# Kernel tuning notes

Measured on AMD Instinct MI355X. Metric: run time of the kernel, lower is better.

The kernel has to match this reference:

```python
import jax, jax.numpy as jnp
import numpy as np

IGNORE_INDEX = -100


def setup_inputs() -> dict:
    key = jax.random.key(0)
    k1, k2, k3 = jax.random.split(key, 3)
    N, H, V = 4096, 1024, 32000
    x = jax.random.normal(k1, (N, H), dtype=jnp.float32)
    # lm_head weight, laid out [H, V] so logits = x @ weight (kernel's [D, V] layout)
    weight = jax.random.normal(k2, (H, V), dtype=jnp.float32) * (1.0 / np.sqrt(H))
    target = jax.random.randint(k3, (N,), 0, V)
    # exercise the ignore_index masking path
    target = target.at[:64].set(IGNORE_INDEX)
    return {"x": x, "weight": weight, "target": target}


def reference(x, weight, target):
    # Fused linear + cross entropy, reduction='sum'.
    # logits: [N, V] (the tensor the fused kernel tiles to avoid materializing)
    logits = jnp.dot(x, weight)
    lse = jax.nn.logsumexp(logits, axis=-1)                  # [N]
    valid = target != IGNORE_INDEX                            # [N]
    safe_labels = jnp.where(valid, target, 0)
    target_logits = jnp.take_along_axis(logits, safe_labels[:, None], axis=-1)[:, 0]
    vmask = valid.astype(logits.dtype)
    losses = (lse - target_logits) * vmask                    # [N], 0 where ignored
    lse_masked = lse * vmask
    # reduction == 'sum'
    return losses.sum(), lse_masked.sum()
```

## Files before the change

### kernel.cpp

```cpp
#include <hip/hip_runtime.h>
#include <hip/hip_bf16.h>

typedef float f32x4 __attribute__((ext_vector_type(4)));
typedef int i32x4v __attribute__((ext_vector_type(4)));
typedef int i32x8v __attribute__((ext_vector_type(8)));

#define IGNORE_INDEX (-100)
#define N_ROWS 4096
#define H_DIM  1024
#define V_DIM  32000

#define BM 128
#define BN 128
#define BK 128
#define CT_NUM (V_DIM / BN)
#define RT_NUM (N_ROWS / BM)
#define SCALE1 0x7f7f7f7f

#define XB8 (N_ROWS * H_DIM / (256 * 16))
__global__ __launch_bounds__(256) void k_prep(const float* __restrict__ x,
                                              const float* __restrict__ w,
                                              unsigned char* __restrict__ x8,
                                              unsigned char* __restrict__ wT8) {
  __shared__ float tile[128][65];
  const int t = threadIdx.x;
  if (blockIdx.x < XB8) {
    size_t i = ((size_t)blockIdx.x * 256 + t) * 16;
    const float4* xp = (const float4*)(x + i);
    float4 f0 = xp[0], f1 = xp[1], f2 = xp[2], f3 = xp[3];
    int4 o;
    int r;
    r = __builtin_amdgcn_cvt_pk_fp8_f32(f0.x, f0.y, 0, false);
    r = __builtin_amdgcn_cvt_pk_fp8_f32(f0.z, f0.w, r, true);
    o.x = r;
    r = __builtin_amdgcn_cvt_pk_fp8_f32(f1.x, f1.y, 0, false);
    r = __builtin_amdgcn_cvt_pk_fp8_f32(f1.z, f1.w, r, true);
    o.y = r;
    r = __builtin_amdgcn_cvt_pk_fp8_f32(f2.x, f2.y, 0, false);
    r = __builtin_amdgcn_cvt_pk_fp8_f32(f2.z, f2.w, r, true);
    o.z = r;
    r = __builtin_amdgcn_cvt_pk_fp8_f32(f3.x, f3.y, 0, false);
    r = __builtin_amdgcn_cvt_pk_fp8_f32(f3.z, f3.w, r, true);
    o.w = r;
    *(int4*)(x8 + i) = o;
    return;
  }
  const int b = blockIdx.x - XB8;
  const int v0 = (b % (V_DIM / 64)) * 64;
  const int k0 = (b / (V_DIM / 64)) * 128;
  {
    const int vq = t & 15;
    const int kr = t >> 4;
#pragma unroll
    for (int p = 0; p < 128; p += 16) {
      float4 v = *(const float4*)(w + (size_t)(k0 + kr + p) * V_DIM + v0 + vq * 4);
      tile[kr + p][vq * 4 + 0] = v.x;
      tile[kr + p][vq * 4 + 1] = v.y;
      tile[kr + p][vq * 4 + 2] = v.z;
      tile[kr + p][vq * 4 + 3] = v.w;
    }
  }
  __syncthreads();
  {
    const int vr = t >> 2;
    const int kq2 = t & 3;
#pragma unroll
    for (int h = 0; h < 2; ++h) {
      const int d4 = kq2 + h * 4;
      int4 o;
      int r;
#pragma unroll
      for (int d = 0; d < 4; ++d) {
        r = __builtin_amdgcn_cvt_pk_fp8_f32(tile[d4 * 16 + d * 4 + 0][vr],
                                            tile[d4 * 16 + d * 4 + 1][vr], 0, false);
        r = __builtin_amdgcn_cvt_pk_fp8_f32(tile[d4 * 16 + d * 4 + 2][vr],
                                            tile[d4 * 16 + d * 4 + 3][vr], r, true);
        ((int*)&o)[d] = r;
      }
      *(int4*)(wT8 + (size_t)(v0 + vr) * H_DIM + k0 + d4 * 16) = o;
    }
  }
}

__global__ __launch_bounds__(256) void k_gemm_lse(const unsigned char* __restrict__ A,
                                                  const unsigned char* __restrict__ Bt,
                                                  float* __restrict__ m_part,
                                                  float* __restrict__ s_part) {
  __shared__ __align__(16) unsigned char sMem[2][2][BM * BK];
  float* maxbuf = (float*)&sMem[0][0][0];
  float* sumbuf = (float*)&sMem[0][0][2048];

  const int tid = threadIdx.x;
  const int rt = blockIdx.x;
  const int ct = blockIdx.y;
  const int m0 = rt * BM;
  const int n0 = ct * BN;

  const int w = tid >> 6;
  const int l = tid & 63;
  const int wr = w >> 1, wc = w & 1;
  const int quad = l >> 4, lc = l & 15;

  f32x4 acc[4][4];
#pragma unroll
  for (int i = 0; i < 4; ++i)
#pragma unroll
    for (int j = 0; j < 4; ++j)
      acc[i][j] = (f32x4){0.f, 0.f, 0.f, 0.f};

  const int srow = tid >> 3;
  const int scol = ((tid & 7) ^ ((tid >> 3) & 7)) * 16;
  const unsigned char* ga = A + (size_t)(m0 + srow) * H_DIM + scol;
  const unsigned char* gb = Bt + (size_t)(n0 + srow) * H_DIM + scol;
  const int dOff = tid * 16;

  const int base_r = lc * 128;
  const int sw0 = ((quad * 2) ^ (lc & 7)) * 16;
  const int sw1 = ((quad * 2 + 1) ^ (lc & 7)) * 16;

#define ISSUE_TILE(buf)                                                          \
  do {                                                                           \
    unsigned char* da_ = &sMem[buf][0][dOff];                                    \
    unsigned char* db_ = &sMem[buf][1][dOff];                                    \
    _Pragma("unroll")                                                            \
    for (int i_ = 0; i_ < 4; ++i_) {                                             \
      __builtin_amdgcn_global_load_lds(                                          \
          (const __attribute__((address_space(1))) void*)(ga + (size_t)i_ * 32 * H_DIM), \
          (__attribute__((address_space(3))) void*)(da_ + i_ * 4096), 16, 0, 0); \
      __builtin_amdgcn_global_load_lds(                                          \
          (const __attribute__((address_space(1))) void*)(gb + (size_t)i_ * 32 * H_DIM), \
          (__attribute__((address_space(3))) void*)(db_ + i_ * 4096), 16, 0, 0); \
    }                                                                            \
    ga += BK;                                                                    \
    gb += BK;                                                                    \
  } while (0)

  ISSUE_TILE(0);

#pragma unroll
  for (int kt = 0; kt < H_DIM / BK; ++kt) {
    __syncthreads();
    if (kt < H_DIM / BK - 1) ISSUE_TILE((kt + 1) & 1);

    const unsigned char* bufA = &sMem[kt & 1][0][0];
    const unsigned char* bufB = &sMem[kt & 1][1][0];
    i32x8v a_frag[4], b_frag[4];
#pragma unroll
    for (int i = 0; i < 4; ++i) {
      const unsigned char* p = bufA + (wr * 4 + i) * 2048 + base_r;
      i32x4v lo = *(const i32x4v*)(p + sw0);
      i32x4v hi = *(const i32x4v*)(p + sw1);
      a_frag[i] = __builtin_shufflevector(lo, hi, 0, 1, 2, 3, 4, 5, 6, 7);
    }
#pragma unroll
    for (int j = 0; j < 4; ++j) {
      const unsigned char* p = bufB + (wc * 4 + j) * 2048 + base_r;
      i32x4v lo = *(const i32x4v*)(p + sw0);
      i32x4v hi = *(const i32x4v*)(p + sw1);
      b_frag[j] = __builtin_shufflevector(lo, hi, 0, 1, 2, 3, 4, 5, 6, 7);
    }
#pragma unroll
    for (int i = 0; i < 4; ++i)
#pragma unroll
      for (int j = 0; j < 4; ++j)
        acc[i][j] = __builtin_amdgcn_mfma_scale_f32_16x16x128_f8f6f4(
            a_frag[i], b_frag[j], acc[i][j], 0, 0, 0, SCALE1, 0, SCALE1);
  }
#undef ISSUE_TILE

  float rmax[4][4];
#pragma unroll
  for (int i = 0; i < 4; ++i)
#pragma unroll
    for (int r = 0; r < 4; ++r) {
      float mx = fmaxf(fmaxf(acc[i][0][r], acc[i][1][r]),
                       fmaxf(acc[i][2][r], acc[i][3][r]));
#pragma unroll
      for (int off = 1; off < 16; off <<= 1)
        mx = fmaxf(mx, __shfl_xor(mx, off, 64));
      rmax[i][r] = mx;
    }
  __syncthreads();
  if (lc == 0) {
#pragma unroll
    for (int i = 0; i < 4; ++i)
#pragma unroll
      for (int r = 0; r < 4; ++r)
        maxbuf[(wr * 64 + i * 16 + quad * 4 + r) * 2 + wc] = rmax[i][r];
  }
  __syncthreads();
  float rowmax[4][4];
#pragma unroll
  for (int i = 0; i < 4; ++i)
#pragma unroll
    for (int r = 0; r < 4; ++r) {
      int row = wr * 64 + i * 16 + quad * 4 + r;
      rowmax[i][r] = fmaxf(maxbuf[row * 2], maxbuf[row * 2 + 1]);
    }
#pragma unroll
  for (int i = 0; i < 4; ++i)
#pragma unroll
    for (int r = 0; r < 4; ++r) {
      float s = __expf(acc[i][0][r] - rowmax[i][r]) + __expf(acc[i][1][r] - rowmax[i][r]) +
                __expf(acc[i][2][r] - rowmax[i][r]) + __expf(acc[i][3][r] - rowmax[i][r]);
#pragma unroll
      for (int off = 1; off < 16; off <<= 1)
        s += __shfl_xor(s, off, 64);
      if (lc == 0) sumbuf[(wr * 64 + i * 16 + quad * 4 + r) * 2 + wc] = s;
    }
  __syncthreads();
  if (wc == 0 && lc == 0) {
#pragma unroll
    for (int i = 0; i < 4; ++i)
#pragma unroll
      for (int r = 0; r < 4; ++r) {
        int row = wr * 64 + i * 16 + quad * 4 + r;
        size_t idx = (size_t)(m0 + row) * CT_NUM + ct;
        m_part[idx] = rowmax[i][r];
        s_part[idx] = sumbuf[row * 2] + sumbuf[row * 2 + 1];
      }
  }
}

__global__ __launch_bounds__(256) void k_combine(const float* __restrict__ x,
                                                 const unsigned char* __restrict__ wT8,
                                                 const int* __restrict__ target,
                                                 const float* __restrict__ m_part,
                                                 const float* __restrict__ s_part,
                                                 float* __restrict__ blk_part) {
  __shared__ float red[8];
  const int wv = threadIdx.x >> 6;
  const int row = blockIdx.x * 4 + wv;
  const int l = threadIdx.x & 63;
  float m = -INFINITY, s = 0.f;
  for (int ctb = l; ctb < CT_NUM; ctb += 64) {
    float mj = m_part[(size_t)row * CT_NUM + ctb];
    float sj = s_part[(size_t)row * CT_NUM + ctb];
    float M = fmaxf(m, mj);
    s = s * __expf(m - M) + sj * __expf(mj - M);
    m = M;
  }
#pragma unroll
  for (int off = 1; off < 64; off <<= 1) {
    float mo = __shfl_xor(m, off, 64);
    float so = __shfl_xor(s, off, 64);
    float M = fmaxf(m, mo);
    s = s * __expf(m - M) + so * __expf(mo - M);
    m = M;
  }
  float lse = m + logf(s);
  int tgt = target[row];
  bool valid = (tgt != IGNORE_INDEX);
  int st = valid ? tgt : 0;
  const float* xr = x + (size_t)row * H_DIM + l * 16;
  int4 wv4 = *(const int4*)(wT8 + (size_t)st * H_DIM + l * 16);
  float t = 0.f;
#define ACC_DW(dw, base)                                              \
  t += xr[base + 0] * __builtin_amdgcn_cvt_f32_fp8(dw, 0);            \
  t += xr[base + 1] * __builtin_amdgcn_cvt_f32_fp8(dw, 1);            \
  t += xr[base + 2] * __builtin_amdgcn_cvt_f32_fp8(dw, 2);            \
  t += xr[base + 3] * __builtin_amdgcn_cvt_f32_fp8(dw, 3);
  ACC_DW(wv4.x, 0)
  ACC_DW(wv4.y, 4)
  ACC_DW(wv4.z, 8)
  ACC_DW(wv4.w, 12)
#undef ACC_DW
#pragma unroll
  for (int off = 1; off < 64; off <<= 1)
    t += __shfl_xor(t, off, 64);
  if (l == 0) {
    red[wv * 2]     = valid ? (lse - t) : 0.f;
    red[wv * 2 + 1] = valid ? lse : 0.f;
  }
  __syncthreads();
  if (threadIdx.x == 0) {
    blk_part[blockIdx.x * 2]     = red[0] + red[2] + red[4] + red[6];
    blk_part[blockIdx.x * 2 + 1] = red[1] + red[3] + red[5] + red[7];
  }
}

__global__ __launch_bounds__(256) void k_final(const float* __restrict__ bp,
                                               float* __restrict__ out) {
  __shared__ float ra[4], rb[4];
  float a = 0.f, b = 0.f;
  for (int i = threadIdx.x; i < N_ROWS / 4; i += 256) {
    a += bp[i * 2];
    b += bp[i * 2 + 1];
  }
#pragma unroll
  for (int off = 1; off < 64; off <<= 1) {
    a += __shfl_xor(a, off, 64);
    b += __shfl_xor(b, off, 64);
  }
  if ((threadIdx.x & 63) == 0) { ra[threadIdx.x >> 6] = a; rb[threadIdx.x >> 6] = b; }
  __syncthreads();
  if (threadIdx.x == 0) {
    out[0] = ra[0] + ra[1] + ra[2] + ra[3];
    out[1] = rb[0] + rb[1] + rb[2] + rb[3];
  }
}

extern "C" void kernel_launch(void* const* d_in, const int* in_sizes, int n_in,
                              void* d_out, int out_size, void* d_ws, size_t ws_size,
                              hipStream_t stream) {
  const float* x = (const float*)d_in[0];
  const float* w = (const float*)d_in[1];
  const int* target = (const int*)d_in[2];
  float* out = (float*)d_out;

  char* ws = (char*)d_ws;
  unsigned char* x8 = (unsigned char*)ws;
  unsigned char* wT8 = (unsigned char*)(ws + 4194304);
  float* m_part = (float*)(ws + 4194304 + 32768000);
  float* s_part = (float*)(ws + 4194304 + 32768000 + 4096000);
  float* blk_part = (float*)(ws + 4194304 + 32768000 + 4096000 + 4096000);

  k_prep<<<dim3(XB8 + (V_DIM / 64) * (H_DIM / 128)), 256, 0, stream>>>(x, w, x8, wT8);
  k_gemm_lse<<<dim3(RT_NUM, CT_NUM), 256, 0, stream>>>(x8, wT8, m_part, s_part);
  k_combine<<<dim3(N_ROWS / 4), 256, 0, stream>>>(x, wT8, target, m_part, s_part, blk_part);
  k_final<<<dim3(1), 256, 0, stream>>>(blk_part, out);
}
```

Before: 434.2 us.

## Enlarge GEMM tiles to 256x256 with 16-wave blocks and fold final reduction into atomics

The FP8 GEMM+LSE kernel moves from 128x128 to 256x256 output tiles. Each block now has 1024 threads in a 4x4 wave grid, and the cross-wave max/sum reductions are resized to match. This roughly doubles operand reuse per LDS byte and halves the number of partial LSE entries, at the cost of 128KB LDS and one resident block per CU. Separately, the single-block final reduction kernel is replaced by per-block atomicAdds into a memset output, which removes one launch but makes the summation order nondeterministic.

Measured after the change: 617.2 us. 1.42x slower.

```diff
diff --git a/kernel.cpp b/kernel.cpp
--- a/kernel.cpp
+++ b/kernel.cpp
@@ -10,8 +10,8 @@
 #define H_DIM  1024
 #define V_DIM  32000
 
-#define BM 128
-#define BN 128
+#define BM 256
+#define BN 256
 #define BK 128
 #define CT_NUM (V_DIM / BN)
 #define RT_NUM (N_ROWS / BM)
@@ -82,13 +82,13 @@
   }
 }
 
-__global__ __launch_bounds__(256) void k_gemm_lse(const unsigned char* __restrict__ A,
-                                                  const unsigned char* __restrict__ Bt,
-                                                  float* __restrict__ m_part,
-                                                  float* __restrict__ s_part) {
+__global__ __launch_bounds__(1024, 1) void k_gemm_lse(const unsigned char* __restrict__ A,
+                                                      const unsigned char* __restrict__ Bt,
+                                                      float* __restrict__ m_part,
+                                                      float* __restrict__ s_part) {
   __shared__ __align__(16) unsigned char sMem[2][2][BM * BK];
   float* maxbuf = (float*)&sMem[0][0][0];
-  float* sumbuf = (float*)&sMem[0][0][2048];
+  float* sumbuf = (float*)&sMem[0][0][4096];
 
   const int tid = threadIdx.x;
   const int rt = blockIdx.x;
@@ -98,7 +98,8 @@
 
   const int w = tid >> 6;
   const int l = tid & 63;
-  const int wr = w >> 1, wc = w & 1;
+  const int wr = w >> 2;
+  const int wc = w & 3;
   const int quad = l >> 4, lc = l & 15;
 
   f32x4 acc[4][4];
@@ -123,13 +124,13 @@
     unsigned char* da_ = &sMem[buf][0][dOff];                                    \
     unsigned char* db_ = &sMem[buf][1][dOff];                                    \
     _Pragma("unroll")                                                            \
-    for (int i_ = 0; i_ < 4; ++i_) {                                             \
+    for (int i_ = 0; i_ < 2; ++i_) {                                             \
       __builtin_amdgcn_global_load_lds(                                          \
-          (const __attribute__((address_space(1))) void*)(ga + (size_t)i_ * 32 * H_DIM), \
-          (__attribute__((address_space(3))) void*)(da_ + i_ * 4096), 16, 0, 0); \
+          (const __attribute__((address_space(1))) void*)(ga + (size_t)i_ * 128 * H_DIM), \
+          (__attribute__((address_space(3))) void*)(da_ + i_ * 16384), 16, 0, 0);\
       __builtin_amdgcn_global_load_lds(                                          \
-          (const __attribute__((address_space(1))) void*)(gb + (size_t)i_ * 32 * H_DIM), \
-          (__attribute__((address_space(3))) void*)(db_ + i_ * 4096), 16, 0, 0); \
+          (const __attribute__((address_space(1))) void*)(gb + (size_t)i_ * 128 * H_DIM), \
+          (__attribute__((address_space(3))) void*)(db_ + i_ * 16384), 16, 0, 0);\
     }                                                                            \
     ga += BK;                                                                    \
     gb += BK;                                                                    \
@@ -186,7 +187,7 @@
     for (int i = 0; i < 4; ++i)
 #pragma unroll
       for (int r = 0; r < 4; ++r)
-        maxbuf[(wr * 64 + i * 16 + quad * 4 + r) * 2 + wc] = rmax[i][r];
+        maxbuf[(wr * 64 + i * 16 + quad * 4 + r) * 4 + wc] = rmax[i][r];
   }
   __syncthreads();
   float rowmax[4][4];
@@ -195,7 +196,8 @@
 #pragma unroll
     for (int r = 0; r < 4; ++r) {
       int row = wr * 64 + i * 16 + quad * 4 + r;
-      rowmax[i][r] = fmaxf(maxbuf[row * 2], maxbuf[row * 2 + 1]);
+      rowmax[i][r] = fmaxf(fmaxf(maxbuf[row * 4], maxbuf[row * 4 + 1]),
+                           fmaxf(maxbuf[row * 4 + 2], maxbuf[row * 4 + 3]));
     }
 #pragma unroll
   for (int i = 0; i < 4; ++i)
@@ -206,7 +208,7 @@
 #pragma unroll
       for (int off = 1; off < 16; off <<= 1)
         s += __shfl_xor(s, off, 64);
-      if (lc == 0) sumbuf[(wr * 64 + i * 16 + quad * 4 + r) * 2 + wc] = s;
+      if (lc == 0) sumbuf[(wr * 64 + i * 16 + quad * 4 + r) * 4 + wc] = s;
     }
   __syncthreads();
   if (wc == 0 && lc == 0) {
@@ -217,7 +219,8 @@
         int row = wr * 64 + i * 16 + quad * 4 + r;
         size_t idx = (size_t)(m0 + row) * CT_NUM + ct;
         m_part[idx] = rowmax[i][r];
-        s_part[idx] = sumbuf[row * 2] + sumbuf[row * 2 + 1];
+        s_part[idx] = sumbuf[row * 4] + sumbuf[row * 4 + 1] +
+                      sumbuf[row * 4 + 2] + sumbuf[row * 4 + 3];
       }
   }
 }
@@ -227,7 +230,7 @@
                                                  const int* __restrict__ target,
                                                  const float* __restrict__ m_part,
                                                  const float* __restrict__ s_part,
-                                                 float* __restrict__ blk_part) {
+                                                 float* __restrict__ out) {
   __shared__ float red[8];
   const int wv = threadIdx.x >> 6;
   const int row = blockIdx.x * 4 + wv;
@@ -274,29 +277,8 @@
   }
   __syncthreads();
   if (threadIdx.x == 0) {
-    blk_part[blockIdx.x * 2]     = red[0] + red[2] + red[4] + red[6];
-    blk_part[blockIdx.x * 2 + 1] = red[1] + red[3] + red[5] + red[7];
-  }
-}
-
-__global__ __launch_bounds__(256) void k_final(const float* __restrict__ bp,
-                                               float* __restrict__ out) {
-  __shared__ float ra[4], rb[4];
-  float a = 0.f, b = 0.f;
-  for (int i = threadIdx.x; i < N_ROWS / 4; i += 256) {
-    a += bp[i * 2];
-    b += bp[i * 2 + 1];
-  }
-#pragma unroll
-  for (int off = 1; off < 64; off <<= 1) {
-    a += __shfl_xor(a, off, 64);
-    b += __shfl_xor(b, off, 64);
-  }
-  if ((threadIdx.x & 63) == 0) { ra[threadIdx.x >> 6] = a; rb[threadIdx.x >> 6] = b; }
-  __syncthreads();
-  if (threadIdx.x == 0) {
-    out[0] = ra[0] + ra[1] + ra[2] + ra[3];
-    out[1] = rb[0] + rb[1] + rb[2] + rb[3];
+    atomicAdd(&out[0], red[0] + red[2] + red[4] + red[6]);
+    atomicAdd(&out[1], red[1] + red[3] + red[5] + red[7]);
   }
 }
 
@@ -312,11 +294,10 @@
   unsigned char* x8 = (unsigned char*)ws;
   unsigned char* wT8 = (unsigned char*)(ws + 4194304);
   float* m_part = (float*)(ws + 4194304 + 32768000);
-  float* s_part = (float*)(ws + 4194304 + 32768000 + 4096000);
-  float* blk_part = (float*)(ws + 4194304 + 32768000 + 4096000 + 4096000);
-
+  float* s_part = (float*)(ws + 4194304 + 32768000 + 2048000);
+
+  hipMemsetAsync(d_out, 0, (size_t)out_size * sizeof(float), stream);
   k_prep<<<dim3(XB8 + (V_DIM / 64) * (H_DIM / 128)), 256, 0, stream>>>(x, w, x8, wT8);
-  k_gemm_lse<<<dim3(RT_NUM, CT_NUM), 256, 0, stream>>>(x8, wT8, m_part, s_part);
-  k_combine<<<dim3(N_ROWS / 4), 256, 0, stream>>>(x, wT8, target, m_part, s_part, blk_part);
-  k_final<<<dim3(1), 256, 0, stream>>>(blk_part, out);
+  k_gemm_lse<<<dim3(RT_NUM, CT_NUM), 1024, 0, stream>>>(x8, wT8, m_part, s_part);
+  k_combine<<<dim3(N_ROWS / 4), 256, 0, stream>>>(x, wT8, target, m_part, s_part, out);
 }
```
